# Performance work log

Hardware: AMD Instinct MI355X
Metric: run time of the kernel (lower is better)

## Reference

```python
import jax, jax.numpy as jnp
import numpy as np

B, T, F, H = 512, 512, 64, 64  # batch, time, input feat, hidden


def setup_inputs() -> dict:
    key = jax.random.key(0)
    k1, k2, k3, k4 = jax.random.split(key, 4)
    ins = jax.random.normal(k1, (B, T, F), jnp.float32)
    resets = jax.random.randint(k2, (B, T), 0, 2).astype(bool)
    # Flax LSTMCell: 4 input->hidden dense (no bias) + 4 hidden->hidden dense (bias),
    # concatenated here as [i, f, g, o] blocks of width H.
    si = 1.0 / np.sqrt(F)
    sh = 1.0 / np.sqrt(H)
    Wi = jax.random.uniform(k3, (F, 4 * H), jnp.float32, -si, si)
    Wh = jax.random.uniform(k4, (H, 4 * H), jnp.float32, -sh, sh)
    b = jnp.zeros((4 * H,), jnp.float32)
    return {"ins": ins, "resets": resets, "Wi": Wi, "Wh": Wh, "b": b}


def reference(ins, resets, Wi, Wh, b):
    Bn, Tn, _ = ins.shape
    Hn = Wh.shape[0]

    def step(carry, xt):
        c, h = carry
        x_t, r_t = xt  # x_t: [B, F], r_t: [B]
        m = r_t[:, None]
        c = jnp.where(m, 0.0, c)  # reset to initialize_carry (zeros)
        h = jnp.where(m, 0.0, h)
        z = x_t @ Wi + h @ Wh + b  # [B, 4H]
        i, f, g, o = jnp.split(z, 4, axis=-1)
        i = jax.nn.sigmoid(i)
        f = jax.nn.sigmoid(f)
        g = jnp.tanh(g)
        o = jax.nn.sigmoid(o)
        c_new = f * c + i * g
        h_new = o * jnp.tanh(c_new)
        return (c_new, h_new), h_new

    c0 = jnp.zeros((Bn, Hn), ins.dtype)
    h0 = jnp.zeros((Bn, Hn), ins.dtype)
    xs = (jnp.swapaxes(ins, 0, 1), jnp.swapaxes(resets, 0, 1))  # time-major
    _, ys = jax.lax.scan(step, (c0, h0), xs)
    return jnp.swapaxes(ys, 0, 1)  # [B, T, H]
```

## Files before the change

kernel.cpp:

```cpp
#include <hip/hip_runtime.h>


#define NB 512
#define NT 512
#define NF 64
#define NH 64
#define NG 256
#define TCHUNK 32

__device__ __forceinline__ float rcp_fast(float x) { return __builtin_amdgcn_rcpf(x); }
__device__ __forceinline__ float sig_fast(float x) { return rcp_fast(1.0f + __expf(-x)); }
__device__ __forceinline__ float tanh_fast(float x) {
    return 1.0f - 2.0f * rcp_fast(1.0f + __expf(2.0f * x));
}

__global__ void detect_resets_dtype(const unsigned int* __restrict__ r, int n,
                                    int* __restrict__ flag) {
    int bits = 0;
    for (int i = blockIdx.x * blockDim.x + threadIdx.x; i < n;
         i += gridDim.x * blockDim.x) {
        unsigned v = r[i];
        if (v == 0x3F800000u) bits |= 2;
        else if (v != 0u && v != 1u) bits |= 4;
    }
    if (bits) atomicOr(flag, bits);
}

__global__ __launch_bounds__(256, 2)
void lstm_scan_kernel(const float* __restrict__ ins, const void* __restrict__ resets,
                      const float* __restrict__ Wi, const float* __restrict__ Wh,
                      const float* __restrict__ bias, float* __restrict__ out,
                      const int* __restrict__ flag) {
    const int b = blockIdx.x;
    const int j = threadIdx.x;

    int mode = 0;
    if (flag) {
        int fl = *flag;
        if ((fl & 2) && !(fl & 4)) mode = 2;
        else if (fl & 4) mode = 1;
    }

    float wi[NF], wh[NF];
#pragma unroll
    for (int k = 0; k < NF; ++k) {
        wi[k] = Wi[k * NG + j];
        wh[k] = Wh[k * NG + j];
    }
    const float bj = bias[j];

    __shared__ __align__(16) float xs[TCHUNK][NF];
    __shared__ int rs[TCHUNK];
    __shared__ __align__(16) float hbuf[2][NH];
    __shared__ float zbuf[NG];

    float c = 0.0f;
    if (j < NH) { hbuf[0][j] = 0.0f; hbuf[1][j] = 0.0f; }
    __syncthreads();

    int cur = 0;
    for (int t0 = 0; t0 < NT; t0 += TCHUNK) {
        {
            const float4* src = (const float4*)(ins + ((size_t)b * NT + t0) * NF);
            float4* dst = (float4*)&xs[0][0];
            dst[j] = src[j];
            dst[j + 256] = src[j + 256];
            if (j < TCHUNK) {
                int idx = b * NT + t0 + j;
                int rv;
                if (mode == 1)      rv = ((const unsigned char*)resets)[idx] != 0;
                else if (mode == 2) rv = ((const float*)resets)[idx] != 0.0f;
                else                rv = ((const int*)resets)[idx] != 0;
                rs[j] = rv;
            }
        }
        __syncthreads();

        for (int tt = 0; tt < TCHUNK; ++tt) {
            const int t = t0 + tt;
            const int rst = rs[tt];

            float accx = bj;
            float acch = 0.0f;
            const float4* xv4 = (const float4*)&xs[tt][0];
#pragma unroll
            for (int k4 = 0; k4 < NF / 4; ++k4) {
                float4 xv = xv4[k4];
                accx = fmaf(xv.x, wi[4 * k4 + 0], accx);
                accx = fmaf(xv.y, wi[4 * k4 + 1], accx);
                accx = fmaf(xv.z, wi[4 * k4 + 2], accx);
                accx = fmaf(xv.w, wi[4 * k4 + 3], accx);
            }
            if (!rst) {
                const float4* hv4 = (const float4*)&hbuf[cur][0];
#pragma unroll
                for (int k4 = 0; k4 < NF / 4; ++k4) {
                    float4 hv = hv4[k4];
                    acch = fmaf(hv.x, wh[4 * k4 + 0], acch);
                    acch = fmaf(hv.y, wh[4 * k4 + 1], acch);
                    acch = fmaf(hv.z, wh[4 * k4 + 2], acch);
                    acch = fmaf(hv.w, wh[4 * k4 + 3], acch);
                }
            }
            zbuf[j] = accx + acch;
            __syncthreads();

            if (j < NH) {
                float zi = zbuf[j];
                float zf = zbuf[j + NH];
                float zg = zbuf[j + 2 * NH];
                float zo = zbuf[j + 3 * NH];
                float ig = sig_fast(zi);
                float fg = sig_fast(zf);
                float gg = tanh_fast(zg);
                float og = sig_fast(zo);
                float cc = rst ? 0.0f : c;
                cc = fg * cc + ig * gg;
                c = cc;
                float hh = og * tanh_fast(cc);
                hbuf[cur ^ 1][j] = hh;
                out[((size_t)b * NT + t) * NH + j] = hh;
            }
            __syncthreads();
            cur ^= 1;
        }
    }
}

extern "C" void kernel_launch(void* const* d_in, const int* in_sizes, int n_in,
                              void* d_out, int out_size, void* d_ws, size_t ws_size,
                              hipStream_t stream) {
    const float* ins    = (const float*)d_in[0];
    const void*  resets = d_in[1];
    const float* Wi     = (const float*)d_in[2];
    const float* Wh     = (const float*)d_in[3];
    const float* bias   = (const float*)d_in[4];
    float* out = (float*)d_out;

    int* flag = nullptr;
    if (d_ws && ws_size >= sizeof(int)) {
        flag = (int*)d_ws;
        hipMemsetAsync(flag, 0, sizeof(int), stream);
        detect_resets_dtype<<<256, 256, 0, stream>>>(
            (const unsigned int*)resets, NB * NT, flag);
    }

    lstm_scan_kernel<<<NB, 256, 0, stream>>>(ins, resets, Wi, Wh, bias, out, flag);
}
```

Before: 495.8 us.

## Hoist input projection into bf16 MFMA GEMM and run wave-local recurrence

Splits the LSTM into two stages. First, an MFMA bf16 GEMM precomputes x@Wi+b for all timesteps into the workspace, with a gate-interleaved layout so each lane's four gates sit together. Second, a single-wave-per-batch recurrence keeps all of Wh in registers, broadcasts h with readlane and needs no block barriers. This removes the per-step input matvec and the syncthreads from the serial loop, at the cost of a large intermediate Z buffer (fp32 or bf16), bf16 rounding of inputs and weights, and heavy register pressure. Which path runs depends on workspace size, and the original kernel remains as a fallback.

```diff
diff --git a/kernel.cpp b/kernel.cpp
--- a/kernel.cpp
+++ b/kernel.cpp
@@ -1,5 +1,8 @@
 #include <hip/hip_runtime.h>
 
+
+typedef __attribute__((ext_vector_type(8))) short short8;
+typedef __attribute__((ext_vector_type(4))) float f32x4;
 
 #define NB 512
 #define NT 512
@@ -12,6 +15,11 @@
 __device__ __forceinline__ float sig_fast(float x) { return rcp_fast(1.0f + __expf(-x)); }
 __device__ __forceinline__ float tanh_fast(float x) {
     return 1.0f - 2.0f * rcp_fast(1.0f + __expf(2.0f * x));
+}
+__device__ __forceinline__ unsigned short f2bf(float x) {
+    unsigned u = __float_as_uint(x);
+    unsigned r = (u + 0x7FFFu + ((u >> 16) & 1u)) >> 16;
+    return (unsigned short)r;
 }
 
 __global__ void detect_resets_dtype(const unsigned int* __restrict__ r, int n,
@@ -26,6 +34,167 @@
     if (bits) atomicOr(flag, bits);
 }
 
+__device__ __forceinline__ int decode_mode(const int* flag) {
+    int fl = *flag;
+    if ((fl & 2) && !(fl & 4)) return 2;
+    if (fl & 4) return 1;
+    return 0;
+}
+__device__ __forceinline__ int load_rst(const void* resets, int mode, long idx) {
+    if (mode == 1) return ((const unsigned char*)resets)[idx] != 0;
+    if (mode == 2) return ((const float*)resets)[idx] != 0.0f;
+    return ((const int*)resets)[idx] != 0;
+}
+
+template<int ZBF>
+__global__ __launch_bounds__(256, 2)
+void zgemm_kernel(const float* __restrict__ ins, const float* __restrict__ Wi,
+                  const float* __restrict__ bias, void* __restrict__ Zv) {
+    const int lane = threadIdx.x & 63;
+    const int w    = threadIdx.x >> 6;
+    const int l15  = lane & 15;
+    const int l4   = lane >> 4;
+    const long bt0 = (long)blockIdx.x * 64;
+    const int pbase = w * 64;
+
+    short8 afr[4][2];
+    f32x4  binit[4];
+#pragma unroll
+    for (int pt = 0; pt < 4; ++pt) {
+        const int prow = pbase + pt * 16 + l15;
+        const int n = (prow & 3) * 64 + (prow >> 2);
+#pragma unroll
+        for (int kc = 0; kc < 2; ++kc) {
+            short8 f;
+#pragma unroll
+            for (int e = 0; e < 8; ++e) {
+                const int k = kc * 32 + l4 * 8 + e;
+                f[e] = (short)f2bf(Wi[k * NG + n]);
+            }
+            afr[pt][kc] = f;
+        }
+        f32x4 bi;
+#pragma unroll
+        for (int r = 0; r < 4; ++r) {
+            const int pr = pbase + pt * 16 + l4 * 4 + r;
+            const int n2 = (pr & 3) * 64 + (pr >> 2);
+            bi[r] = bias[n2];
+        }
+        binit[pt] = bi;
+    }
+
+#pragma unroll
+    for (int tt = 0; tt < 4; ++tt) {
+        const long bt = bt0 + tt * 16 + l15;
+        short8 bfr[2];
+#pragma unroll
+        for (int kc = 0; kc < 2; ++kc) {
+            const float4* xp = (const float4*)(ins + bt * NF + kc * 32 + l4 * 8);
+            float4 v0 = xp[0];
+            float4 v1 = xp[1];
+            short8 f;
+            f[0] = (short)f2bf(v0.x); f[1] = (short)f2bf(v0.y);
+            f[2] = (short)f2bf(v0.z); f[3] = (short)f2bf(v0.w);
+            f[4] = (short)f2bf(v1.x); f[5] = (short)f2bf(v1.y);
+            f[6] = (short)f2bf(v1.z); f[7] = (short)f2bf(v1.w);
+            bfr[kc] = f;
+        }
+#pragma unroll
+        for (int pt = 0; pt < 4; ++pt) {
+            f32x4 acc = binit[pt];
+            acc = __builtin_amdgcn_mfma_f32_16x16x32_bf16(afr[pt][0], bfr[0], acc, 0, 0, 0);
+            acc = __builtin_amdgcn_mfma_f32_16x16x32_bf16(afr[pt][1], bfr[1], acc, 0, 0, 0);
+            const int p0 = pbase + pt * 16 + l4 * 4;
+            if (ZBF) {
+                unsigned lo = (unsigned)f2bf(acc[0]) | ((unsigned)f2bf(acc[1]) << 16);
+                unsigned hi = (unsigned)f2bf(acc[2]) | ((unsigned)f2bf(acc[3]) << 16);
+                uint2* dst = (uint2*)((unsigned short*)Zv + bt * NG + p0);
+                *dst = make_uint2(lo, hi);
+            } else {
+                f32x4* dst = (f32x4*)((float*)Zv + bt * NG + p0);
+                *dst = acc;
+            }
+        }
+    }
+}
+
+template<int ZBF>
+__global__ __launch_bounds__(64, 1)
+void lstm_recur_kernel(const void* __restrict__ Zv, const void* __restrict__ resets,
+                       const float* __restrict__ Wh, float* __restrict__ out,
+                       const int* __restrict__ flag) {
+    const int b = blockIdx.x;
+    const int j = threadIdx.x;
+    const int mode = decode_mode(flag);
+
+    float whi[NF], whf[NF], whg[NF], who[NF];
+#pragma unroll
+    for (int k = 0; k < NF; ++k) {
+        whi[k] = Wh[k * NG + j];
+        whf[k] = Wh[k * NG + NH + j];
+        whg[k] = Wh[k * NG + 2 * NH + j];
+        who[k] = Wh[k * NG + 3 * NH + j];
+    }
+
+    float h = 0.0f, c = 0.0f;
+    const long base = (long)b * NT;
+
+    float z0, z1, z2, z3;
+    {
+        if (ZBF) {
+            const uint2 zz = *(const uint2*)((const unsigned short*)Zv + base * NG + j * 4);
+            z0 = __uint_as_float(zz.x << 16);
+            z1 = __uint_as_float(zz.x & 0xFFFF0000u);
+            z2 = __uint_as_float(zz.y << 16);
+            z3 = __uint_as_float(zz.y & 0xFFFF0000u);
+        } else {
+            const f32x4 zz = *(const f32x4*)((const float*)Zv + base * NG + j * 4);
+            z0 = zz[0]; z1 = zz[1]; z2 = zz[2]; z3 = zz[3];
+        }
+    }
+    int rc = load_rst(resets, mode, base);
+
+    for (int t = 0; t < NT; ++t) {
+        const long tn = base + (t + 1 < NT ? t + 1 : NT - 1);
+        float n0, n1, n2, n3;
+        if (ZBF) {
+            const uint2 zz = *(const uint2*)((const unsigned short*)Zv + tn * NG + j * 4);
+            n0 = __uint_as_float(zz.x << 16);
+            n1 = __uint_as_float(zz.x & 0xFFFF0000u);
+            n2 = __uint_as_float(zz.y << 16);
+            n3 = __uint_as_float(zz.y & 0xFFFF0000u);
+        } else {
+            const f32x4 zz = *(const f32x4*)((const float*)Zv + tn * NG + j * 4);
+            n0 = zz[0]; n1 = zz[1]; n2 = zz[2]; n3 = zz[3];
+        }
+        const int rn = load_rst(resets, mode, tn);
+
+        float zi = z0, zf = z1, zg = z2, zo = z3;
+        if (!rc) {
+#pragma unroll
+            for (int k = 0; k < NF; ++k) {
+                const float hk = __uint_as_float(
+                    (unsigned)__builtin_amdgcn_readlane(__float_as_uint(h), k));
+                zi = fmaf(hk, whi[k], zi);
+                zf = fmaf(hk, whf[k], zf);
+                zg = fmaf(hk, whg[k], zg);
+                zo = fmaf(hk, who[k], zo);
+            }
+        }
+        const float ig = sig_fast(zi);
+        const float fg = sig_fast(zf);
+        const float gg = tanh_fast(zg);
+        const float og = sig_fast(zo);
+        const float cm = rc ? 0.0f : c;
+        c = fmaf(fg, cm, ig * gg);
+        h = og * tanh_fast(c);
+        out[(base + t) * NH + j] = h;
+
+        z0 = n0; z1 = n1; z2 = n2; z3 = n3;
+        rc = rn;
+    }
+}
+
 __global__ __launch_bounds__(256, 2)
 void lstm_scan_kernel(const float* __restrict__ ins, const void* __restrict__ resets,
                       const float* __restrict__ Wi, const float* __restrict__ Wh,
@@ -33,13 +202,7 @@
                       const int* __restrict__ flag) {
     const int b = blockIdx.x;
     const int j = threadIdx.x;
-
-    int mode = 0;
-    if (flag) {
-        int fl = *flag;
-        if ((fl & 2) && !(fl & 4)) mode = 2;
-        else if (fl & 4) mode = 1;
-    }
+    int mode = flag ? decode_mode(flag) : 0;
 
     float wi[NF], wh[NF];
 #pragma unroll
@@ -65,23 +228,14 @@
             float4* dst = (float4*)&xs[0][0];
             dst[j] = src[j];
             dst[j + 256] = src[j + 256];
-            if (j < TCHUNK) {
-                int idx = b * NT + t0 + j;
-                int rv;
-                if (mode == 1)      rv = ((const unsigned char*)resets)[idx] != 0;
-                else if (mode == 2) rv = ((const float*)resets)[idx] != 0.0f;
-                else                rv = ((const int*)resets)[idx] != 0;
-                rs[j] = rv;
-            }
+            if (j < TCHUNK) rs[j] = load_rst(resets, mode, (long)b * NT + t0 + j);
         }
         __syncthreads();
 
         for (int tt = 0; tt < TCHUNK; ++tt) {
             const int t = t0 + tt;
             const int rst = rs[tt];
-
-            float accx = bj;
-            float acch = 0.0f;
+            float accx = bj, acch = 0.0f;
             const float4* xv4 = (const float4*)&xs[tt][0];
 #pragma unroll
             for (int k4 = 0; k4 < NF / 4; ++k4) {
@@ -104,16 +258,9 @@
             }
             zbuf[j] = accx + acch;
             __syncthreads();
-
             if (j < NH) {
-                float zi = zbuf[j];
-                float zf = zbuf[j + NH];
-                float zg = zbuf[j + 2 * NH];
-                float zo = zbuf[j + 3 * NH];
-                float ig = sig_fast(zi);
-                float fg = sig_fast(zf);
-                float gg = tanh_fast(zg);
-                float og = sig_fast(zo);
+                float zi = zbuf[j], zf = zbuf[j + NH], zg = zbuf[j + 2 * NH], zo = zbuf[j + 3 * NH];
+                float ig = sig_fast(zi), fg = sig_fast(zf), gg = tanh_fast(zg), og = sig_fast(zo);
                 float cc = rst ? 0.0f : c;
                 cc = fg * cc + ig * gg;
                 c = cc;
@@ -137,13 +284,29 @@
     const float* bias   = (const float*)d_in[4];
     float* out = (float*)d_out;
 
-    int* flag = nullptr;
-    if (d_ws && ws_size >= sizeof(int)) {
-        flag = (int*)d_ws;
+    const size_t ZF32  = (size_t)NB * NT * NG * 4;
+    const size_t ZBF16 = ZF32 / 2;
+    const int nBT = NB * NT;
+
+    if (ws_size >= ZF32 + 64) {
+        int* flag = (int*)((char*)d_ws + ZF32);
         hipMemsetAsync(flag, 0, sizeof(int), stream);
-        detect_resets_dtype<<<256, 256, 0, stream>>>(
-            (const unsigned int*)resets, NB * NT, flag);
-    }
-
-    lstm_scan_kernel<<<NB, 256, 0, stream>>>(ins, resets, Wi, Wh, bias, out, flag);
-}
+        detect_resets_dtype<<<256, 256, 0, stream>>>((const unsigned int*)resets, nBT, flag);
+        zgemm_kernel<0><<<nBT / 64, 256, 0, stream>>>(ins, Wi, bias, d_ws);
+        lstm_recur_kernel<0><<<NB, 64, 0, stream>>>(d_ws, resets, Wh, out, flag);
+    } else if (ws_size >= ZBF16 + 64) {
+        int* flag = (int*)((char*)d_ws + ZBF16);
+        hipMemsetAsync(flag, 0, sizeof(int), stream);
+        detect_resets_dtype<<<256, 256, 0, stream>>>((const unsigned int*)resets, nBT, flag);
+        zgemm_kernel<1><<<nBT / 64, 256, 0, stream>>>(ins, Wi, bias, d_ws);
+        lstm_recur_kernel<1><<<NB, 64, 0, stream>>>(d_ws, resets, Wh, out, flag);
+    } else {
+        int* flag = nullptr;
+        if (d_ws && ws_size >= sizeof(int)) {
+            flag = (int*)d_ws;
+            hipMemsetAsync(flag, 0, sizeof(int), stream);
+            detect_resets_dtype<<<256, 256, 0, stream>>>((const unsigned int*)resets, nBT, flag);
+        }
+        lstm_scan_kernel<<<NB, 256, 0, stream>>>(ins, resets, Wi, Wh, bias, out, flag);
+    }
+}
```

Result: slower. 553.6 us (+11.7%).
